# Optimization experiments

Measured on AMD Instinct MI355X. Metric: run time of the kernel, lower is better.

The kernel has to match this reference:

```python
import jax, jax.numpy as jnp
import numpy as np


def setup_inputs() -> dict:
    key = jax.random.key(0)
    k1, k2, k3 = jax.random.split(key, 3)
    x = jax.random.normal(k1, (16, 128, 128, 64), dtype=jnp.float32)
    kernel = jax.random.normal(k2, (3, 3, 64, 128), dtype=jnp.float32) * 0.05
    bias = jax.random.normal(k3, (128,), dtype=jnp.float32) * 0.05
    return {"x": x, "kernel": kernel, "bias": bias}


def reference(x, kernel, bias):
    # Faithful to myconv2d: extract_patches (stride 1, rate 1, SAME) followed by
    # per-out-channel multiply+reduce over the flattened (kh*kw*cin) patch axis,
    # which is mathematically a stride-1 SAME conv2d. Expressed as a direct conv.
    out = jax.lax.conv_general_dilated(
        x, kernel,
        window_strides=(1, 1),
        padding="SAME",
        dimension_numbers=("NHWC", "HWIO", "NHWC"),
    )
    return out + bias  # bias broadcast over channel dim, as in call()
```

## Files before the change

kernel.cpp:

```cpp
#include <hip/hip_runtime.h>


#define HH 128
#define WW 128
#define CIN 64
#define COUT 128

typedef __attribute__((ext_vector_type(8))) short v8s;
typedef __attribute__((ext_vector_type(4))) float v4f;

#define ROW_CHUNKS 1040
#define WS_NEEDED  (9u * CIN * COUT * 2u)

static __device__ __forceinline__ unsigned short f2bf(float f) {
    unsigned int u = __float_as_uint(f);
    unsigned int r = (u + 0x7fffu + ((u >> 16) & 1u)) >> 16;
    return (unsigned short)r;
}

__global__ __launch_bounds__(256) void cvt_w(const float* __restrict__ wgt,
                                             unsigned short* __restrict__ wt) {
    int idx = blockIdx.x * 256 + threadIdx.x;
    if (idx >= 9 * CIN * COUT) return;
    int co  = idx & (COUT - 1);
    int ci  = (idx >> 7) & (CIN - 1);
    int tap = idx >> 13;
    wt[(tap * COUT + co) * CIN + ci] = f2bf(wgt[idx]);
}

__global__ __launch_bounds__(256, 3) void conv_mfma(
    const float* __restrict__ x,
    const unsigned short* __restrict__ wt,
    const float* __restrict__ bias,
    float* __restrict__ out) {
    __shared__ v8s smem[3 * ROW_CHUNKS];

    int bid = blockIdx.x;
    int logical = ((bid & 7) << 8) | (bid >> 3);
    int h = logical & (HH - 1);
    int n = logical >> 7;

    int tid  = threadIdx.x;
    int lane = tid & 63;
    int wid  = tid >> 6;
    int wi = wid >> 1;
    int wj = wid & 1;
    int l15  = lane & 15;
    int quad = lane >> 4;
    int pixelL = wi * 64 + l15;

    if (tid < 48) {
        int row = tid >> 4, k = tid & 15;
        int c = (k < 8) ? k : (1024 + k);
        smem[row * ROW_CHUNKS + c] = (v8s)(short)0;
    }

    #pragma unroll
    for (int dh = 0; dh < 3; ++dh) {
        int ih = h + dh - 1;
        v8s* dst = smem + dh * ROW_CHUNKS;
        if (ih >= 0 && ih < HH) {
            const float* rowf = x + ((size_t)(n * HH + ih)) * WW * CIN;
            #pragma unroll
            for (int k = 0; k < 4; ++k) {
                int c = 8 + tid + (k << 8);
                const float* p = rowf + (size_t)(c - 8) * 8;
                float4 a = *(const float4*)p;
                float4 b = *(const float4*)(p + 4);
                v8s ch;
                ch[0] = (short)f2bf(a.x); ch[1] = (short)f2bf(a.y);
                ch[2] = (short)f2bf(a.z); ch[3] = (short)f2bf(a.w);
                ch[4] = (short)f2bf(b.x); ch[5] = (short)f2bf(b.y);
                ch[6] = (short)f2bf(b.z); ch[7] = (short)f2bf(b.w);
                dst[c ^ ((c >> 3) & 7)] = ch;
            }
        } else {
            #pragma unroll
            for (int k = 0; k < 4; ++k) {
                int c = 8 + tid + (k << 8);
                dst[c ^ ((c >> 3) & 7)] = (v8s)(short)0;
            }
        }
    }
    __syncthreads();

    v4f acc[4][4];
    #pragma unroll
    for (int i = 0; i < 4; ++i)
        #pragma unroll
        for (int j = 0; j < 4; ++j) acc[i][j] = (v4f)0.f;

    const unsigned short* wlane = wt + (wj * 64 + l15) * CIN + quad * 8;
    int abase = pixelL * 8 + quad;

    v8s bcur[4], bnxt[4];
    #pragma unroll
    for (int t = 0; t < 4; ++t)
        bcur[t] = *(const v8s*)(wlane + t * 16 * CIN);

    #pragma unroll
    for (int s = 0; s < 18; ++s) {
        const int tap = s >> 1;
        const int dh  = tap / 3;
        const int dw  = tap % 3;
        const int kc  = s & 1;

        if (s < 17) {
            const int tapn = (s + 1) >> 1;
            const int kcn  = (s + 1) & 1;
            const unsigned short* wp =
                wlane + tapn * (COUT * CIN) + kcn * 32;
            #pragma unroll
            for (int t = 0; t < 4; ++t)
                bnxt[t] = *(const v8s*)(wp + t * 16 * CIN);
        }

        const v8s* srow = smem + dh * ROW_CHUNKS;
        const int sw = (pixelL + dw) & 7;

        v8s a0 = srow[(abase + (0 * 16 + dw) * 8 + kc * 4) ^ sw];
        v8s a1 = srow[(abase + (1 * 16 + dw) * 8 + kc * 4) ^ sw];
        #pragma unroll
        for (int tj = 0; tj < 4; ++tj)
            acc[0][tj] = __builtin_amdgcn_mfma_f32_16x16x32_bf16(
                a0, bcur[tj], acc[0][tj], 0, 0, 0);
        v8s a2 = srow[(abase + (2 * 16 + dw) * 8 + kc * 4) ^ sw];
        #pragma unroll
        for (int tj = 0; tj < 4; ++tj)
            acc[1][tj] = __builtin_amdgcn_mfma_f32_16x16x32_bf16(
                a1, bcur[tj], acc[1][tj], 0, 0, 0);
        v8s a3 = srow[(abase + (3 * 16 + dw) * 8 + kc * 4) ^ sw];
        #pragma unroll
        for (int tj = 0; tj < 4; ++tj)
            acc[2][tj] = __builtin_amdgcn_mfma_f32_16x16x32_bf16(
                a2, bcur[tj], acc[2][tj], 0, 0, 0);
        #pragma unroll
        for (int tj = 0; tj < 4; ++tj)
            acc[3][tj] = __builtin_amdgcn_mfma_f32_16x16x32_bf16(
                a3, bcur[tj], acc[3][tj], 0, 0, 0);

        if (s < 17) {
            #pragma unroll
            for (int t = 0; t < 4; ++t) bcur[t] = bnxt[t];
        }
    }

    float bv[4];
    #pragma unroll
    for (int tj = 0; tj < 4; ++tj) bv[tj] = bias[wj * 64 + tj * 16 + l15];

    float* orow = out + ((size_t)(n * HH + h)) * WW * COUT;
    #pragma unroll
    for (int ti = 0; ti < 4; ++ti) {
        #pragma unroll
        for (int r = 0; r < 4; ++r) {
            int p = wi * 64 + ti * 16 + quad * 4 + r;
            float* op = orow + (size_t)p * COUT + wj * 64 + l15;
            #pragma unroll
            for (int tj = 0; tj < 4; ++tj)
                op[tj * 16] = acc[ti][tj][r] + bv[tj];
        }
    }
}

__global__ __launch_bounds__(256) void conv3x3_direct(
    const float* __restrict__ x, const float* __restrict__ wgt,
    const float* __restrict__ bias, float* __restrict__ out) {
    int idx = blockIdx.x * 256 + threadIdx.x;
    int co = idx & (COUT - 1);
    int w  = (idx >> 7) & (WW - 1);
    int h  = (idx >> 14) & (HH - 1);
    int n  = idx >> 21;
    float acc = bias[co];
    #pragma unroll
    for (int kh = 0; kh < 3; ++kh) {
        int ih = h + kh - 1;
        if (ih < 0 || ih >= HH) continue;
        #pragma unroll
        for (int kw = 0; kw < 3; ++kw) {
            int iw = w + kw - 1;
            if (iw < 0 || iw >= WW) continue;
            const float* xp = x + (((size_t)(n * HH + ih) * WW + iw) * CIN);
            const float* wp = wgt + ((size_t)((kh * 3 + kw) * CIN)) * COUT + co;
            #pragma unroll 8
            for (int ci = 0; ci < CIN; ++ci)
                acc = fmaf(xp[ci], wp[(size_t)ci * COUT], acc);
        }
    }
    out[idx] = acc;
}

extern "C" void kernel_launch(void* const* d_in, const int* in_sizes, int n_in,
                              void* d_out, int out_size, void* d_ws, size_t ws_size,
                              hipStream_t stream) {
    const float* x    = (const float*)d_in[0];
    const float* wgt  = (const float*)d_in[1];
    const float* bias = (const float*)d_in[2];
    float* out = (float*)d_out;

    if (ws_size < (size_t)WS_NEEDED) {
        int blocks = (out_size + 255) / 256;
        conv3x3_direct<<<blocks, 256, 0, stream>>>(x, wgt, bias, out);
        return;
    }

    unsigned short* wt = (unsigned short*)d_ws;
    cvt_w<<<(9 * CIN * COUT + 255) / 256, 256, 0, stream>>>(wgt, wt);
    conv_mfma<<<16 * HH, 256, 0, stream>>>(x, wt, bias, out);
}
```

Before: 248.0 us.

## Repartition warp tiles to 128 pixels by 32 channels with triple-buffered weights

Each of the four warps now computes all 128 output pixels of the row for a 32-channel slice, instead of a 64x64 pixel-by-channel quadrant. The weight workspace is re-laid out per (tap, K-chunk) so each lane's B fragment is contiguous, and weight loads are triple-buffered two steps ahead, with the first loads issued before the barrier. This reduces per-warp global weight traffic and register B fragments but doubles LDS A-fragment reads per warp, which may make LDS bandwidth the limit.

```diff
diff --git a/kernel.cpp b/kernel.cpp
--- a/kernel.cpp
+++ b/kernel.cpp
@@ -25,7 +25,9 @@
     int co  = idx & (COUT - 1);
     int ci  = (idx >> 7) & (CIN - 1);
     int tap = idx >> 13;
-    wt[(tap * COUT + co) * CIN + ci] = f2bf(wgt[idx]);
+    int kc  = ci >> 5;
+    int cl  = ci & 31;
+    wt[((tap * 2 + kc) * COUT + co) * 32 + cl] = f2bf(wgt[idx]);
 }
 
 __global__ __launch_bounds__(256, 3) void conv_mfma(
@@ -43,11 +45,8 @@
     int tid  = threadIdx.x;
     int lane = tid & 63;
     int wid  = tid >> 6;
-    int wi = wid >> 1;
-    int wj = wid & 1;
     int l15  = lane & 15;
     int quad = lane >> 4;
-    int pixelL = wi * 64 + l15;
 
     if (tid < 48) {
         int row = tid >> 4, k = tid & 15;
@@ -82,21 +81,23 @@
             }
         }
     }
+
+    const unsigned short* wlane = wt + ((size_t)(wid * 32 + l15)) * 32 + quad * 8;
+
+    v8s bb[3][2];
+    #pragma unroll
+    for (int tj = 0; tj < 2; ++tj) {
+        bb[0][tj] = *(const v8s*)(wlane + 0 * 4096 + tj * 512);
+        bb[1][tj] = *(const v8s*)(wlane + 1 * 4096 + tj * 512);
+    }
+
     __syncthreads();
 
-    v4f acc[4][4];
-    #pragma unroll
-    for (int i = 0; i < 4; ++i)
-        #pragma unroll
-        for (int j = 0; j < 4; ++j) acc[i][j] = (v4f)0.f;
-
-    const unsigned short* wlane = wt + (wj * 64 + l15) * CIN + quad * 8;
-    int abase = pixelL * 8 + quad;
-
-    v8s bcur[4], bnxt[4];
-    #pragma unroll
-    for (int t = 0; t < 4; ++t)
-        bcur[t] = *(const v8s*)(wlane + t * 16 * CIN);
+    v4f acc[8][2];
+    #pragma unroll
+    for (int i = 0; i < 8; ++i)
+        #pragma unroll
+        for (int j = 0; j < 2; ++j) acc[i][j] = (v4f)0.f;
 
     #pragma unroll
     for (int s = 0; s < 18; ++s) {
@@ -104,61 +105,75 @@
         const int dh  = tap / 3;
         const int dw  = tap % 3;
         const int kc  = s & 1;
-
-        if (s < 17) {
-            const int tapn = (s + 1) >> 1;
-            const int kcn  = (s + 1) & 1;
-            const unsigned short* wp =
-                wlane + tapn * (COUT * CIN) + kcn * 32;
+        const int cur = s % 3;
+
+        if (s < 16) {
+            const int nb = (s + 2) % 3;
             #pragma unroll
-            for (int t = 0; t < 4; ++t)
-                bnxt[t] = *(const v8s*)(wp + t * 16 * CIN);
+            for (int tj = 0; tj < 2; ++tj)
+                bb[nb][tj] = *(const v8s*)(wlane + (s + 2) * 4096 + tj * 512);
         }
 
         const v8s* srow = smem + dh * ROW_CHUNKS;
-        const int sw = (pixelL + dw) & 7;
-
-        v8s a0 = srow[(abase + (0 * 16 + dw) * 8 + kc * 4) ^ sw];
-        v8s a1 = srow[(abase + (1 * 16 + dw) * 8 + kc * 4) ^ sw];
-        #pragma unroll
-        for (int tj = 0; tj < 4; ++tj)
+        const int pl0 = l15 + dw;
+        const int sw  = pl0 & 7;
+        const int c0  = pl0 * 8 + kc * 4 + quad;
+
+        v8s a0 = srow[(c0 + 0 * 128) ^ sw];
+        v8s a1 = srow[(c0 + 1 * 128) ^ sw];
+        #pragma unroll
+        for (int tj = 0; tj < 2; ++tj)
             acc[0][tj] = __builtin_amdgcn_mfma_f32_16x16x32_bf16(
-                a0, bcur[tj], acc[0][tj], 0, 0, 0);
-        v8s a2 = srow[(abase + (2 * 16 + dw) * 8 + kc * 4) ^ sw];
-        #pragma unroll
-        for (int tj = 0; tj < 4; ++tj)
+                a0, bb[cur][tj], acc[0][tj], 0, 0, 0);
+        v8s a2 = srow[(c0 + 2 * 128) ^ sw];
+        #pragma unroll
+        for (int tj = 0; tj < 2; ++tj)
             acc[1][tj] = __builtin_amdgcn_mfma_f32_16x16x32_bf16(
-                a1, bcur[tj], acc[1][tj], 0, 0, 0);
-        v8s a3 = srow[(abase + (3 * 16 + dw) * 8 + kc * 4) ^ sw];
-        #pragma unroll
-        for (int tj = 0; tj < 4; ++tj)
+                a1, bb[cur][tj], acc[1][tj], 0, 0, 0);
+        v8s a3 = srow[(c0 + 3 * 128) ^ sw];
+        #pragma unroll
+        for (int tj = 0; tj < 2; ++tj)
             acc[2][tj] = __builtin_amdgcn_mfma_f32_16x16x32_bf16(
-                a2, bcur[tj], acc[2][tj], 0, 0, 0);
-        #pragma unroll
-        for (int tj = 0; tj < 4; ++tj)
+                a2, bb[cur][tj], acc[2][tj], 0, 0, 0);
+        v8s a4 = srow[(c0 + 4 * 128) ^ sw];
+        #pragma unroll
+        for (int tj = 0; tj < 2; ++tj)
             acc[3][tj] = __builtin_amdgcn_mfma_f32_16x16x32_bf16(
-                a3, bcur[tj], acc[3][tj], 0, 0, 0);
-
-        if (s < 17) {
-            #pragma unroll
-            for (int t = 0; t < 4; ++t) bcur[t] = bnxt[t];
-        }
-    }
-
-    float bv[4];
-    #pragma unroll
-    for (int tj = 0; tj < 4; ++tj) bv[tj] = bias[wj * 64 + tj * 16 + l15];
+                a3, bb[cur][tj], acc[3][tj], 0, 0, 0);
+        v8s a5 = srow[(c0 + 5 * 128) ^ sw];
+        #pragma unroll
+        for (int tj = 0; tj < 2; ++tj)
+            acc[4][tj] = __builtin_amdgcn_mfma_f32_16x16x32_bf16(
+                a4, bb[cur][tj], acc[4][tj], 0, 0, 0);
+        v8s a6 = srow[(c0 + 6 * 128) ^ sw];
+        #pragma unroll
+        for (int tj = 0; tj < 2; ++tj)
+            acc[5][tj] = __builtin_amdgcn_mfma_f32_16x16x32_bf16(
+                a5, bb[cur][tj], acc[5][tj], 0, 0, 0);
+        v8s a7 = srow[(c0 + 7 * 128) ^ sw];
+        #pragma unroll
+        for (int tj = 0; tj < 2; ++tj)
+            acc[6][tj] = __builtin_amdgcn_mfma_f32_16x16x32_bf16(
+                a6, bb[cur][tj], acc[6][tj], 0, 0, 0);
+        #pragma unroll
+        for (int tj = 0; tj < 2; ++tj)
+            acc[7][tj] = __builtin_amdgcn_mfma_f32_16x16x32_bf16(
+                a7, bb[cur][tj], acc[7][tj], 0, 0, 0);
+    }
+
+    float bv[2];
+    #pragma unroll
+    for (int tj = 0; tj < 2; ++tj) bv[tj] = bias[wid * 32 + tj * 16 + l15];
 
     float* orow = out + ((size_t)(n * HH + h)) * WW * COUT;
     #pragma unroll
-    for (int ti = 0; ti < 4; ++ti) {
+    for (int ti = 0; ti < 8; ++ti) {
         #pragma unroll
         for (int r = 0; r < 4; ++r) {
-            int p = wi * 64 + ti * 16 + quad * 4 + r;
-            float* op = orow + (size_t)p * COUT + wj * 64 + l15;
-            #pragma unroll
-            for (int tj = 0; tj < 4; ++tj)
-                op[tj * 16] = acc[ti][tj][r] + bv[tj];
+            int p = ti * 16 + quad * 4 + r;
+            float* op = orow + (size_t)p * COUT + wid * 32 + l15;
+            op[0]  = acc[ti][0][r] + bv[0];
+            op[16] = acc[ti][1][r] + bv[1];
         }
     }
 }
```

Result: faster. 212.3 us (-14.4%).
